# Kernel optimization log

Measured on AMD Instinct MI355X. Metric: run time of the kernel, lower is better.

The kernel has to match this reference:

```python
import jax, jax.numpy as jnp
import numpy as np


def _resize_hw(x, h, w):
    # PyTorch F.interpolate(mode='bilinear', align_corners=False) == half-pixel
    # bilinear without antialiasing.
    return jax.image.resize(x, x.shape[:-2] + (h, w), method='bilinear', antialias=False)


def _make_char_mask(attn, fore_mask, alpha):
    # attn: [b,26,w_attn] float; fore_mask: [b,1,H,W] int32
    W = fore_mask.shape[-1]
    attn_i = _resize_hw(attn[:, None], 26, W)[:, 0]          # [b,26,W]
    attn_b = (attn_i > alpha).astype(jnp.int32)              # threshold
    single = attn_b[:, :, None, :] * fore_mask               # [b,26,H,W]
    return jnp.concatenate([1 - fore_mask, single], axis=1)  # [b,27,H,W]


def _loss(char_feature, mask, length):
    # char_feature: [b,27,H,W] logits; mask: [b,27,H,W] int; length: [b]
    c = char_feature.shape[1]
    target = jnp.argmax(mask, axis=1)                         # [b,H,W] (first-max, same as torch)
    logp = jax.nn.log_softmax(char_feature, axis=1)
    ce = -jnp.mean(jnp.take_along_axis(logp, target[:, None], axis=1))
    prob = jnp.exp(logp)
    m = mask.astype(prob.dtype)
    smooth = 1.0
    inter = jnp.sum(prob * m, axis=(2, 3))                    # [b,27]
    s1 = jnp.sum(prob, axis=(2, 3))
    s2 = jnp.sum(m, axis=(2, 3))
    score = (2.0 * inter + smooth) / (s1 + s2 + smooth)       # [b,27]
    lens = length - 1                                          # chars per sample
    ch = jnp.arange(c)
    valid = (ch[None, :] >= 1) & (ch[None, :] <= lens[:, None])  # channels 1..len
    per_sample = jnp.sum((1.0 - score) * valid, axis=1) / lens.astype(prob.dtype)
    dice = jnp.mean(per_sample)
    return ce + dice


def setup_inputs() -> dict:
    key = jax.random.key(0)
    k1, k2, k3, k4, k5 = jax.random.split(key, 5)
    b = 512
    return {
        'char_feature_mid': jax.random.normal(k1, (b, 27, 32, 128), dtype=jnp.float32),
        'char_feature_low': jax.random.normal(k2, (b, 27, 16, 64), dtype=jnp.float32),
        'seq1_attention_map': jax.random.uniform(k3, (b, 26, 32), dtype=jnp.float32),
        'fore_mask': jax.random.uniform(k4, (b, 1, 32, 128), dtype=jnp.float32),
        'length': jax.random.randint(k5, (b,), 2, 27),
        'alpha': jnp.float32(0.3),
    }


def reference(char_feature_mid, char_feature_low, seq1_attention_map, fore_mask, length, alpha):
    h_mid, w_mid = char_feature_mid.shape[-2:]
    h_low, w_low = char_feature_low.shape[-2:]
    # clear_noise: zero attention rows at index >= length-1
    keep = jnp.arange(seq1_attention_map.shape[1])[None, :] < (length - 1)[:, None]
    attn = seq1_attention_map * keep[..., None].astype(seq1_attention_map.dtype)
    # low-resolution branch
    fm_low = (_resize_hw(fore_mask, h_low, w_low) >= 0.4).astype(jnp.int32)
    mask_low = _make_char_mask(attn, fm_low, alpha)
    loss_low = _loss(char_feature_low, mask_low, length)
    # middle-resolution branch
    fm_mid = (_resize_hw(fore_mask, h_mid, w_mid) >= 0.4).astype(jnp.int32)
    mask_mid = _make_char_mask(attn, fm_mid, alpha)
    loss_middle = _loss(char_feature_mid, mask_mid, length)
    return ((loss_low, loss_middle), mask_low)
```

## Files before the change

kernel.cpp:

```cpp
#include <hip/hip_runtime.h>
#include <stdint.h>


static __device__ __forceinline__ float wave_reduce_add(float v) {
  v += __shfl_xor(v, 1, 64);
  v += __shfl_xor(v, 2, 64);
  v += __shfl_xor(v, 4, 64);
  v += __shfl_xor(v, 8, 64);
  v += __shfl_xor(v, 16, 64);
  v += __shfl_xor(v, 32, 64);
  return v;
}

__global__ void zero_kernel(float* out) {
  if (threadIdx.x < 2) out[threadIdx.x] = 0.0f;
}

template <bool LOW>
__global__ __launch_bounds__(256) void loss_kernel(
    const float* __restrict__ cf,
    const float* __restrict__ attn,
    const float* __restrict__ fore,
    const int* __restrict__ length,
    const float* __restrict__ alpha_p,
    float* __restrict__ out) {
  constexpr int W  = LOW ? 64 : 128;
  constexpr int HW = LOW ? 1024 : 4096;
  constexpr int PX = HW / 256;

  const int b = blockIdx.x;
  const int t = threadIdx.x;

  __shared__ float    sattn[26 * 32];
  __shared__ uint32_t sbits[W];
  __shared__ float    red[4][82];

  for (int i = t; i < 26 * 32; i += 256) sattn[i] = attn[b * 832 + i];
  __syncthreads();

  const float alpha = alpha_p[0];
  const int lens = length[b] - 1;

  if (t < W) {
    const float src = (LOW ? 0.5f : 0.25f) * (float)t - (LOW ? 0.25f : 0.375f);
    const int k0 = (int)floorf(src);
    const float frac = src - (float)k0;
    uint32_t bits = 0u;
    if (k0 < 0 || k0 >= 31) {
      const int kk = (k0 < 0) ? 0 : 31;
      for (int c = 0; c < 26; ++c) {
        float v = (c < lens) ? sattn[c * 32 + kk] : 0.0f;
        if (v > alpha) bits |= (1u << c);
      }
    } else {
      const float w1 = frac, w0 = 1.0f - frac;
      for (int c = 0; c < 26; ++c) {
        float v = __fadd_rn(__fmul_rn(w0, sattn[c * 32 + k0]),
                            __fmul_rn(w1, sattn[c * 32 + k0 + 1]));
        v = (c < lens) ? v : 0.0f;
        if (v > alpha) bits |= (1u << c);
      }
    }
    sbits[t] = bits;
  }
  __syncthreads();

  float inter[27], s1[27], s2[27];
#pragma unroll
  for (int c = 0; c < 27; ++c) { inter[c] = 0.0f; s1[c] = 0.0f; s2[c] = 0.0f; }
  float ce = 0.0f;

  const float* cfb = cf + (size_t)b * 27 * HW;
  float* mout = out + 2 + (size_t)b * 27 * 1024;

  for (int k = 0; k < PX; ++k) {
    const int p = t + k * 256;
    const int x = p & (W - 1);

    int fmw;
    if (LOW) {
      const int y = p >> 6;
      const float2* fr =
          (const float2*)(fore + (size_t)b * 4096 + (size_t)(2 * y) * 128 + 2 * x);
      const float2 f0 = fr[0];
      const float2 f1 = fr[64];
      const float t0 = __fadd_rn(0.5f * f0.x, 0.5f * f1.x);
      const float t1 = __fadd_rn(0.5f * f0.y, 0.5f * f1.y);
      const float fmv = __fadd_rn(0.5f * t0, 0.5f * t1);
      fmw = (fmv >= 0.4f) ? 1 : 0;
    } else {
      fmw = (fore[(size_t)b * 4096 + p] >= 0.4f) ? 1 : 0;
    }

    const uint32_t bits = sbits[x];
    const int target = fmw ? (int)__ffs(bits) : 0;

    float l[27];
    float m = -1e30f;
    float lt = 0.0f;
#pragma unroll
    for (int c = 0; c < 27; ++c) {
      const float v = cfb[(size_t)c * HW + p];
      l[c] = v;
      m = fmaxf(m, v);
      lt = (c == target) ? v : lt;
    }
    float s = 0.0f;
#pragma unroll
    for (int c = 0; c < 27; ++c) {
      const float e = __expf(l[c] - m);
      l[c] = e;
      s += e;
    }
    const float inv = 1.0f / s;
    const float logZ = m + __logf(s);
    ce += (logZ - lt);

#pragma unroll
    for (int c = 0; c < 27; ++c) {
      const float prob = l[c] * inv;
      s1[c] += prob;
      float mf;
      if (c == 0) {
        mf = (float)(1 - fmw);
      } else {
        mf = (float)(((bits >> (c - 1)) & 1u) & (uint32_t)fmw);
      }
      inter[c] += prob * mf;
      s2[c] += mf;
      if (LOW) mout[(size_t)c * 1024 + p] = mf;
    }
  }

  const int wave = t >> 6;
  const int lane = t & 63;
#pragma unroll
  for (int c = 0; c < 27; ++c) {
    inter[c] = wave_reduce_add(inter[c]);
    s1[c] = wave_reduce_add(s1[c]);
    s2[c] = wave_reduce_add(s2[c]);
  }
  ce = wave_reduce_add(ce);
  if (lane == 0) {
#pragma unroll
    for (int c = 0; c < 27; ++c) {
      red[wave][c] = inter[c];
      red[wave][27 + c] = s1[c];
      red[wave][54 + c] = s2[c];
    }
    red[wave][81] = ce;
  }
  __syncthreads();

  if (t == 0) {
    const float ces = red[0][81] + red[1][81] + red[2][81] + red[3][81];
    float dice = 0.0f;
    for (int c = 1; c < 27; ++c) {
      const float I  = red[0][c] + red[1][c] + red[2][c] + red[3][c];
      const float S1 = red[0][27 + c] + red[1][27 + c] + red[2][27 + c] + red[3][27 + c];
      const float S2 = red[0][54 + c] + red[1][54 + c] + red[2][54 + c] + red[3][54 + c];
      const float score = (2.0f * I + 1.0f) / (S1 + S2 + 1.0f);
      if (c <= lens) dice += (1.0f - score);
    }
    dice /= (float)lens;
    const float contrib =
        dice * (1.0f / 512.0f) + ces * (1.0f / (512.0f * (float)HW));
    atomicAdd(&out[LOW ? 0 : 1], contrib);
  }
}

extern "C" void kernel_launch(void* const* d_in, const int* in_sizes, int n_in,
                              void* d_out, int out_size, void* d_ws, size_t ws_size,
                              hipStream_t stream) {
  const float* cf_mid = (const float*)d_in[0];
  const float* cf_low = (const float*)d_in[1];
  const float* attn   = (const float*)d_in[2];
  const float* fore   = (const float*)d_in[3];
  const int*   length = (const int*)d_in[4];
  const float* alpha  = (const float*)d_in[5];
  float* out = (float*)d_out;

  hipLaunchKernelGGL(zero_kernel, dim3(1), dim3(64), 0, stream, out);
  hipLaunchKernelGGL((loss_kernel<true>), dim3(512), dim3(256), 0, stream,
                     cf_low, attn, fore, length, alpha, out);
  hipLaunchKernelGGL((loss_kernel<false>), dim3(512), dim3(256), 0, stream,
                     cf_mid, attn, fore, length, alpha, out);
}
```

Measured before the change: 413.3 us.

## Split per-sample loss into prep, pixel-chunk main, and final reduction kernels

Attention-bit computation moves into a separate prep kernel that writes per-column bitmasks to workspace. The main kernel merges the low and mid branches into one launch of 5120 blocks, each handling 512 pixels of one sample. Per-sample partial sums go into workspace with atomics, and a final kernel computes the dice and CE terms. The aim is more parallelism than one block per sample gives, at the cost of extra launches, workspace traffic and many atomics.

```diff
diff --git a/kernel.cpp b/kernel.cpp
--- a/kernel.cpp
+++ b/kernel.cpp
@@ -12,76 +12,99 @@
   return v;
 }
 
-__global__ void zero_kernel(float* out) {
-  if (threadIdx.x < 2) out[threadIdx.x] = 0.0f;
-}
-
-template <bool LOW>
-__global__ __launch_bounds__(256) void loss_kernel(
-    const float* __restrict__ cf,
+static __device__ __forceinline__ uint32_t attn_bits(const float* sattn, float src,
+                                                     int lens, float alpha) {
+  const int k0 = (int)floorf(src);
+  uint32_t bits = 0u;
+  if (k0 < 0 || k0 >= 31) {
+    const int kk = (k0 < 0) ? 0 : 31;
+    for (int c = 0; c < 26; ++c) {
+      float v = (c < lens) ? sattn[c * 32 + kk] : 0.0f;
+      if (v > alpha) bits |= (1u << c);
+    }
+  } else {
+    const float frac = src - (float)k0;
+    const float w1 = frac, w0 = 1.0f - frac;
+    for (int c = 0; c < 26; ++c) {
+      float v = __fadd_rn(__fmul_rn(w0, sattn[c * 32 + k0]),
+                          __fmul_rn(w1, sattn[c * 32 + k0 + 1]));
+      v = (c < lens) ? v : 0.0f;
+      if (v > alpha) bits |= (1u << c);
+    }
+  }
+  return bits;
+}
+
+__global__ __launch_bounds__(192) void prep_kernel(
     const float* __restrict__ attn,
-    const float* __restrict__ fore,
     const int* __restrict__ length,
     const float* __restrict__ alpha_p,
-    float* __restrict__ out) {
-  constexpr int W  = LOW ? 64 : 128;
-  constexpr int HW = LOW ? 1024 : 4096;
-  constexpr int PX = HW / 256;
-
+    uint32_t* __restrict__ bits_mid,
+    uint32_t* __restrict__ bits_low,
+    float* __restrict__ acc_mid,
+    float* __restrict__ acc_low,
+    float* __restrict__ ce) {
+  __shared__ float sattn[26 * 32];
   const int b = blockIdx.x;
   const int t = threadIdx.x;
-
-  __shared__ float    sattn[26 * 32];
-  __shared__ uint32_t sbits[W];
-  __shared__ float    red[4][82];
-
-  for (int i = t; i < 26 * 32; i += 256) sattn[i] = attn[b * 832 + i];
+  for (int i = t; i < 832; i += 192) sattn[i] = attn[b * 832 + i];
+  if (t < 81) { acc_mid[b * 81 + t] = 0.0f; acc_low[b * 81 + t] = 0.0f; }
+  if (b == 0 && t >= 96 && t < 98) ce[t - 96] = 0.0f;
   __syncthreads();
-
   const float alpha = alpha_p[0];
   const int lens = length[b] - 1;
-
-  if (t < W) {
-    const float src = (LOW ? 0.5f : 0.25f) * (float)t - (LOW ? 0.25f : 0.375f);
-    const int k0 = (int)floorf(src);
-    const float frac = src - (float)k0;
-    uint32_t bits = 0u;
-    if (k0 < 0 || k0 >= 31) {
-      const int kk = (k0 < 0) ? 0 : 31;
-      for (int c = 0; c < 26; ++c) {
-        float v = (c < lens) ? sattn[c * 32 + kk] : 0.0f;
-        if (v > alpha) bits |= (1u << c);
-      }
-    } else {
-      const float w1 = frac, w0 = 1.0f - frac;
-      for (int c = 0; c < 26; ++c) {
-        float v = __fadd_rn(__fmul_rn(w0, sattn[c * 32 + k0]),
-                            __fmul_rn(w1, sattn[c * 32 + k0 + 1]));
-        v = (c < lens) ? v : 0.0f;
-        if (v > alpha) bits |= (1u << c);
-      }
-    }
-    sbits[t] = bits;
-  }
-  __syncthreads();
+  if (t < 128) {
+    const float src = 0.25f * (float)t - 0.375f;
+    bits_mid[b * 128 + t] = attn_bits(sattn, src, lens, alpha);
+  } else {
+    const int x = t - 128;
+    const float src = 0.5f * (float)x - 0.25f;
+    bits_low[b * 64 + x] = attn_bits(sattn, src, lens, alpha);
+  }
+}
+
+__global__ __launch_bounds__(256) void main_kernel(
+    const float* __restrict__ cf_mid,
+    const float* __restrict__ cf_low,
+    const float* __restrict__ fore,
+    float* __restrict__ out,
+    const uint32_t* __restrict__ bits_mid,
+    const uint32_t* __restrict__ bits_low,
+    float* __restrict__ acc_mid,
+    float* __restrict__ acc_low,
+    float* __restrict__ ce) {
+  const int t = threadIdx.x;
+  const int bid = blockIdx.x;
+  const bool low = (bid >= 4096);
+  int b, p0, W, HW;
+  const float* cf;
+  const uint32_t* bitsp;
+  float* acc;
+  if (low) {
+    const int idx = bid - 4096;
+    b = idx >> 1; p0 = (idx & 1) << 9; W = 64; HW = 1024;
+    cf = cf_low; bitsp = bits_low + (size_t)b * 64; acc = acc_low;
+  } else {
+    b = bid >> 3; p0 = (bid & 7) << 9; W = 128; HW = 4096;
+    cf = cf_mid; bitsp = bits_mid + (size_t)b * 128; acc = acc_mid;
+  }
+  const float* cfb = cf + (size_t)b * 27 * HW;
+  const float* fb = fore + (size_t)b * 4096;
+  float* mout = out + 2 + (size_t)b * 27 * 1024;
 
   float inter[27], s1[27], s2[27];
 #pragma unroll
   for (int c = 0; c < 27; ++c) { inter[c] = 0.0f; s1[c] = 0.0f; s2[c] = 0.0f; }
-  float ce = 0.0f;
-
-  const float* cfb = cf + (size_t)b * 27 * HW;
-  float* mout = out + 2 + (size_t)b * 27 * 1024;
-
-  for (int k = 0; k < PX; ++k) {
-    const int p = t + k * 256;
+  float cesum = 0.0f;
+
+  for (int k = 0; k < 2; ++k) {
+    const int p = p0 + t + (k << 8);
     const int x = p & (W - 1);
 
     int fmw;
-    if (LOW) {
+    if (low) {
       const int y = p >> 6;
-      const float2* fr =
-          (const float2*)(fore + (size_t)b * 4096 + (size_t)(2 * y) * 128 + 2 * x);
+      const float2* fr = (const float2*)(fb + (size_t)(2 * y) * 128 + 2 * x);
       const float2 f0 = fr[0];
       const float2 f1 = fr[64];
       const float t0 = __fadd_rn(0.5f * f0.x, 0.5f * f1.x);
@@ -89,15 +112,14 @@
       const float fmv = __fadd_rn(0.5f * t0, 0.5f * t1);
       fmw = (fmv >= 0.4f) ? 1 : 0;
     } else {
-      fmw = (fore[(size_t)b * 4096 + p] >= 0.4f) ? 1 : 0;
-    }
-
-    const uint32_t bits = sbits[x];
+      fmw = (fb[p] >= 0.4f) ? 1 : 0;
+    }
+
+    const uint32_t bits = bitsp[x];
     const int target = fmw ? (int)__ffs(bits) : 0;
 
     float l[27];
-    float m = -1e30f;
-    float lt = 0.0f;
+    float m = -1e30f, lt = 0.0f;
 #pragma unroll
     for (int c = 0; c < 27; ++c) {
       const float v = cfb[(size_t)c * HW + p];
@@ -113,34 +135,30 @@
       s += e;
     }
     const float inv = 1.0f / s;
-    const float logZ = m + __logf(s);
-    ce += (logZ - lt);
+    cesum += (m + __logf(s) - lt);
 
 #pragma unroll
     for (int c = 0; c < 27; ++c) {
       const float prob = l[c] * inv;
       s1[c] += prob;
       float mf;
-      if (c == 0) {
-        mf = (float)(1 - fmw);
-      } else {
-        mf = (float)(((bits >> (c - 1)) & 1u) & (uint32_t)fmw);
-      }
+      if (c == 0) mf = (float)(1 - fmw);
+      else mf = (float)(((bits >> (c - 1)) & 1u) & (uint32_t)fmw);
       inter[c] += prob * mf;
       s2[c] += mf;
-      if (LOW) mout[(size_t)c * 1024 + p] = mf;
-    }
-  }
-
-  const int wave = t >> 6;
-  const int lane = t & 63;
+      if (low) mout[(size_t)c * 1024 + p] = mf;
+    }
+  }
+
+  __shared__ float red[4][82];
+  const int wave = t >> 6, lane = t & 63;
 #pragma unroll
   for (int c = 0; c < 27; ++c) {
     inter[c] = wave_reduce_add(inter[c]);
     s1[c] = wave_reduce_add(s1[c]);
     s2[c] = wave_reduce_add(s2[c]);
   }
-  ce = wave_reduce_add(ce);
+  cesum = wave_reduce_add(cesum);
   if (lane == 0) {
 #pragma unroll
     for (int c = 0; c < 27; ++c) {
@@ -148,24 +166,46 @@
       red[wave][27 + c] = s1[c];
       red[wave][54 + c] = s2[c];
     }
-    red[wave][81] = ce;
+    red[wave][81] = cesum;
   }
   __syncthreads();
-
+  if (t < 82) {
+    const float v = red[0][t] + red[1][t] + red[2][t] + red[3][t];
+    if (t == 81) atomicAdd(&ce[low ? 0 : 1], v);
+    else atomicAdd(&acc[(size_t)b * 81 + t], v);
+  }
+}
+
+__global__ __launch_bounds__(256) void final_kernel(
+    const float* __restrict__ acc_mid,
+    const float* __restrict__ acc_low,
+    const float* __restrict__ ce,
+    const int* __restrict__ length,
+    float* __restrict__ out) {
+  const int B = blockIdx.x;
+  const float* acc = (B == 0) ? acc_low : acc_mid;
+  const float hw = (B == 0) ? 1024.0f : 4096.0f;
+  const int t = threadIdx.x;
+  float dsum = 0.0f;
+  for (int b = t; b < 512; b += 256) {
+    const int lens = length[b] - 1;
+    const float* a = acc + (size_t)b * 81;
+    float d = 0.0f;
+    for (int c = 1; c < 27; ++c) {
+      const float I = a[c], S1 = a[27 + c], S2 = a[54 + c];
+      const float score = (2.0f * I + 1.0f) / (S1 + S2 + 1.0f);
+      if (c <= lens) d += (1.0f - score);
+    }
+    dsum += d / (float)lens;
+  }
+  __shared__ float red[4];
+  const int wave = t >> 6, lane = t & 63;
+  dsum = wave_reduce_add(dsum);
+  if (lane == 0) red[wave] = dsum;
+  __syncthreads();
   if (t == 0) {
-    const float ces = red[0][81] + red[1][81] + red[2][81] + red[3][81];
-    float dice = 0.0f;
-    for (int c = 1; c < 27; ++c) {
-      const float I  = red[0][c] + red[1][c] + red[2][c] + red[3][c];
-      const float S1 = red[0][27 + c] + red[1][27 + c] + red[2][27 + c] + red[3][27 + c];
-      const float S2 = red[0][54 + c] + red[1][54 + c] + red[2][54 + c] + red[3][54 + c];
-      const float score = (2.0f * I + 1.0f) / (S1 + S2 + 1.0f);
-      if (c <= lens) dice += (1.0f - score);
-    }
-    dice /= (float)lens;
-    const float contrib =
-        dice * (1.0f / 512.0f) + ces * (1.0f / (512.0f * (float)HW));
-    atomicAdd(&out[LOW ? 0 : 1], contrib);
+    const float dice = red[0] + red[1] + red[2] + red[3];
+    out[B] = dice * (1.0f / 512.0f) + ce[B] * (1.0f / (512.0f * hw));
   }
 }
 
@@ -180,9 +220,17 @@
   const float* alpha  = (const float*)d_in[5];
   float* out = (float*)d_out;
 
-  hipLaunchKernelGGL(zero_kernel, dim3(1), dim3(64), 0, stream, out);
-  hipLaunchKernelGGL((loss_kernel<true>), dim3(512), dim3(256), 0, stream,
-                     cf_low, attn, fore, length, alpha, out);
-  hipLaunchKernelGGL((loss_kernel<false>), dim3(512), dim3(256), 0, stream,
-                     cf_mid, attn, fore, length, alpha, out);
-}
+  uint32_t* bits_mid = (uint32_t*)d_ws;
+  uint32_t* bits_low = bits_mid + 512 * 128;
+  float* acc_mid = (float*)(bits_low + 512 * 64);
+  float* acc_low = acc_mid + 512 * 81;
+  float* ce = acc_low + 512 * 81;
+
+  hipLaunchKernelGGL(prep_kernel, dim3(512), dim3(192), 0, stream,
+                     attn, length, alpha, bits_mid, bits_low, acc_mid, acc_low, ce);
+  hipLaunchKernelGGL(main_kernel, dim3(5120), dim3(256), 0, stream,
+                     cf_mid, cf_low, fore, out, bits_mid, bits_low,
+                     acc_mid, acc_low, ce);
+  hipLaunchKernelGGL(final_kernel, dim3(2), dim3(256), 0, stream,
+                     acc_mid, acc_low, ce, length, out);
+}
```

New measurement: 411.0 us. Within noise of the previous version (-0.6%).
